# Performance work log

Measured on AMD Instinct MI355X. Metric: run time of the kernel, lower is better.

## Reference

```python
import jax, jax.numpy as jnp
import numpy as np

BS, H = 2048, 1024
XDIM = 2048 + 4 * 64  # x + R*W = 2304
IN = XDIM + 2 * H     # 4352


def setup_inputs() -> dict:
    key = jax.random.key(0)
    ks = jax.random.split(key, 11)
    s = 1.0 / np.sqrt(IN)  # torch Linear default init scale
    return {
        "input_x": jax.random.normal(ks[0], (BS, XDIM), jnp.float32),
        "previous_time": jax.random.normal(ks[1], (BS, H), jnp.float32),
        "previous_layer": jax.random.normal(ks[2], (BS, H), jnp.float32),
        "old_state": jnp.zeros((BS, H), jnp.float32),
        "Wi": jax.random.normal(ks[3], (H, IN), jnp.float32) * s,
        "bi": jax.random.normal(ks[4], (H,), jnp.float32) * s,
        "Wf": jax.random.normal(ks[5], (H, IN), jnp.float32) * s,
        "bf": jax.random.normal(ks[6], (H,), jnp.float32) * s,
        "Wo": jax.random.normal(ks[7], (H, IN), jnp.float32) * s,
        "bo": jax.random.normal(ks[8], (H,), jnp.float32) * s,
        "Ws": jax.random.normal(ks[9], (H, IN), jnp.float32) * s,
        "bs_state": jax.random.normal(ks[10], (H,), jnp.float32) * s,
    }


def reference(input_x, previous_time, previous_layer, old_state,
              Wi, bi, Wf, bf, Wo, bo, Ws, bs_state):
    # semicolon_input: [bs, x + R*W + 2h]
    z = jnp.concatenate([input_x, previous_time, previous_layer], axis=1)
    # Fuse the four projections into one GEMM: [bs, 4h]
    W_all = jnp.concatenate([Wi, Wf, Wo, Ws], axis=0)          # [4h, IN]
    b_all = jnp.concatenate([bi, bf, bo, bs_state], axis=0)    # [4h]
    proj = z @ W_all.T + b_all
    gi, gf, go, gs = jnp.split(proj, 4, axis=1)
    input_gate = jax.nn.sigmoid(gi)
    forget_gate = jax.nn.sigmoid(gf)
    output_gate = jax.nn.sigmoid(go)
    new_state = forget_gate * old_state + input_gate * jnp.tanh(gs)
    new_hidden = output_gate * jnp.tanh(new_state)
    return new_hidden
```

## Files before the change

kernel.cpp:

```cpp
#include <hip/hip_runtime.h>
#include <stdint.h>
#include <stddef.h>

#define M_DIM 2048
#define N_DIM 4096
#define K_DIM 4352
#define H_DIM 1024
#define X_DIM 2304

#define A_OFF 0u
#define B_OFF 17825792u

typedef __bf16 bf16x8 __attribute__((ext_vector_type(8)));
typedef float f32x4 __attribute__((ext_vector_type(4)));

__device__ __forceinline__ unsigned short f32_to_bf16(float f) {
    unsigned u = __float_as_uint(f);
    u += 0x7FFFu + ((u >> 16) & 1u);
    return (unsigned short)(u >> 16);
}

__device__ __forceinline__ float sigm_(float x) { return 1.f / (1.f + __expf(-x)); }
__device__ __forceinline__ float tanh_(float x) {
    x = fminf(15.f, fmaxf(-15.f, x));
    float e = __expf(2.f * x);
    return (e - 1.f) / (e + 1.f);
}

__global__ __launch_bounds__(256) void convert_kernel(
    const float* __restrict__ x, const float* __restrict__ pt,
    const float* __restrict__ pl,
    const float* __restrict__ Wi, const float* __restrict__ Wf,
    const float* __restrict__ Wo, const float* __restrict__ Ws,
    unsigned short* __restrict__ Abf, unsigned short* __restrict__ Bbf)
{
    const int row = blockIdx.x;
    const float* srow = nullptr;
    unsigned short* drow;
    if (row < M_DIM) {
        drow = Abf + (size_t)row * K_DIM;
    } else {
        int n = row - M_DIM;
        int g = n >> 10, h = n & 1023;
        const float* W = (g == 0) ? Wi : (g == 1) ? Wf : (g == 2) ? Wo : Ws;
        srow = W + (size_t)h * K_DIM;
        drow = Bbf + (size_t)(h * 4 + g) * K_DIM;
    }

    for (int c8 = threadIdx.x; c8 < K_DIM / 8; c8 += 256) {
        int col = c8 * 8;
        const float* s;
        if (row < M_DIM) {
            if (col < X_DIM)              s = x  + (size_t)row * X_DIM + col;
            else if (col < X_DIM + H_DIM) s = pt + (size_t)row * H_DIM + (col - X_DIM);
            else                          s = pl + (size_t)row * H_DIM + (col - X_DIM - H_DIM);
        } else {
            s = srow + col;
        }
        float4 v0 = ((const float4*)s)[0];
        float4 v1 = ((const float4*)s)[1];
        union { unsigned short h[8]; uint4 u; } r;
        r.h[0] = f32_to_bf16(v0.x); r.h[1] = f32_to_bf16(v0.y);
        r.h[2] = f32_to_bf16(v0.z); r.h[3] = f32_to_bf16(v0.w);
        r.h[4] = f32_to_bf16(v1.x); r.h[5] = f32_to_bf16(v1.y);
        r.h[6] = f32_to_bf16(v1.z); r.h[7] = f32_to_bf16(v1.w);
        *(uint4*)(drow + col) = r.u;
    }
}

__global__ __launch_bounds__(256) void gemm_fused(
    const unsigned short* __restrict__ A,
    const unsigned short* __restrict__ B,
    const float* __restrict__ old_state,
    const float* __restrict__ bi, const float* __restrict__ bfv,
    const float* __restrict__ bo, const float* __restrict__ bs,
    float* __restrict__ out)
{
    __shared__ __align__(16) char smem[65536];
    float* sP = (float*)smem;

    const int tid  = threadIdx.x;
    const int lane = tid & 63;
    const int wave = tid >> 6;
    const int wm = (wave >> 1) * 64;
    const int wn = (wave & 1) * 64;

    const int b   = blockIdx.x;
    const int xcd = b & 7;
    const int j   = b >> 3;
    const int n0  = (xcd * 4 + (j & 3)) * 128;
    const int m0  = (j >> 2) * 128;

    const int srow = wave * 8 + (lane >> 3);
    const int c8s  = ((lane & 7) ^ (lane >> 3)) * 8;

    const int fr  = lane & 15;
    const int sw  = fr & 7;
    const int kb0 = lane >> 4;

    f32x4 acc[4][4];
#pragma unroll
    for (int i = 0; i < 4; ++i)
#pragma unroll
        for (int jj = 0; jj < 4; ++jj) acc[i][jj] = (f32x4){0.f, 0.f, 0.f, 0.f};

    const unsigned short* Aw = A + (size_t)(m0 + srow) * K_DIM + c8s;
    const unsigned short* Bw = B + (size_t)(n0 + srow) * K_DIM + c8s;

    auto stage = [&](int kt, int bufOff) {
#pragma unroll
        for (int i = 0; i < 4; ++i) {
            __builtin_amdgcn_global_load_lds(
                (const __attribute__((address_space(1))) unsigned*)(Aw + (size_t)i * 32 * K_DIM + kt),
                (__attribute__((address_space(3))) unsigned*)(smem + bufOff + i * 4096 + wave * 1024),
                16, 0, 0);
            __builtin_amdgcn_global_load_lds(
                (const __attribute__((address_space(1))) unsigned*)(Bw + (size_t)i * 32 * K_DIM + kt),
                (__attribute__((address_space(3))) unsigned*)(smem + bufOff + 16384 + i * 4096 + wave * 1024),
                16, 0, 0);
        }
    };

    auto compute = [&](int bufOff) {
        const unsigned short* sA = (const unsigned short*)(smem + bufOff);
        const unsigned short* sB = (const unsigned short*)(smem + bufOff + 16384);
#pragma unroll
        for (int kk = 0; kk < 64; kk += 32) {
            const int kb = kk / 8 + kb0;
            bf16x8 af[4], bfr[4];
#pragma unroll
            for (int i = 0; i < 4; ++i) {
                const int ra  = wm + i * 16 + fr;
                const int rb_ = wn + i * 16 + fr;
                af[i]  = *(const bf16x8*)(sA + (ra  * 8 + (kb ^ sw)) * 8);
                bfr[i] = *(const bf16x8*)(sB + (rb_ * 8 + (kb ^ sw)) * 8);
            }
#pragma unroll
            for (int i = 0; i < 4; ++i)
#pragma unroll
                for (int jj = 0; jj < 4; ++jj)
                    acc[i][jj] = __builtin_amdgcn_mfma_f32_16x16x32_bf16(
                        af[i], bfr[jj], acc[i][jj], 0, 0, 0);
        }
    };

    stage(0, 0);

    for (int kt = 0; kt < K_DIM; kt += 128) {
        __syncthreads();
        if (kt + 64 < K_DIM) stage(kt + 64, 32768);
        compute(0);
        __syncthreads();
        if (kt + 128 < K_DIM) stage(kt + 128, 0);
        compute(32768);
    }

    const int cw = lane & 15;
    const int rw = (lane >> 4) * 4;
    const int hl = tid & 15;
    const int rb = tid >> 4;

    for (int p = 0; p < 2; ++p) {
        __syncthreads();
        if ((wave & 1) == p) {
#pragma unroll
            for (int i = 0; i < 4; ++i)
#pragma unroll
                for (int jj = 0; jj < 4; ++jj)
#pragma unroll
                    for (int r = 0; r < 4; ++r)
                        sP[(wm + i * 16 + rw + r) * 76 + jj * 16 + cw] = acc[i][jj][r];
        }
        __syncthreads();

        const int hg = (n0 >> 2) + p * 16 + hl;
        const float b_i = bi[hg], b_f = bfv[hg], b_o = bo[hg], b_s = bs[hg];
#pragma unroll
        for (int k = 0; k < 8; ++k) {
            const int row = rb + 16 * k;
            float4 g = *(const float4*)(sP + row * 76 + hl * 4);
            const size_t oidx = (size_t)(m0 + row) * H_DIM + hg;
            float old = old_state[oidx];
            float ig = sigm_(g.x + b_i);
            float fg = sigm_(g.y + b_f);
            float og = sigm_(g.z + b_o);
            float ts = tanh_(g.w + b_s);
            out[oidx] = og * tanh_(fg * old + ig * ts);
        }
    }
}

extern "C" void kernel_launch(void* const* d_in, const int* in_sizes, int n_in,
                              void* d_out, int out_size, void* d_ws, size_t ws_size,
                              hipStream_t stream) {
    const float* x   = (const float*)d_in[0];
    const float* pt  = (const float*)d_in[1];
    const float* pl  = (const float*)d_in[2];
    const float* old = (const float*)d_in[3];
    const float* Wi  = (const float*)d_in[4];
    const float* bi  = (const float*)d_in[5];
    const float* Wf  = (const float*)d_in[6];
    const float* bf  = (const float*)d_in[7];
    const float* Wo  = (const float*)d_in[8];
    const float* bo  = (const float*)d_in[9];
    const float* Ws  = (const float*)d_in[10];
    const float* bs  = (const float*)d_in[11];
    float* out = (float*)d_out;

    char* ws = (char*)d_ws;
    unsigned short* Abf = (unsigned short*)(ws + A_OFF);
    unsigned short* Bbf = (unsigned short*)(ws + B_OFF);

    convert_kernel<<<M_DIM + N_DIM, 256, 0, stream>>>(x, pt, pl, Wi, Wf, Wo, Ws, Abf, Bbf);

    gemm_fused<<<512, 256, 0, stream>>>(Abf, Bbf, old, bi, bf, bo, bs, out);
}
```

Measured before the change: 232.9 us.

## Restructure GEMM main loop with explicit waitcnt/barriers, occupancy hint, staggered start

The GEMM main loop now issues the next stage's global-to-LDS loads, then reads all A/B fragments for both k-halves at once and runs the MFMAs, with a manual vmcnt(0) wait and a raw s_barrier in place of __syncthreads. Launch bounds now request two blocks per CU, and half the blocks sleep briefly at start to stagger their memory traffic. The convert kernel switches from 8-wide to 4-wide vectors per thread. Holding all fragments up front raises register pressure, and the manual synchronisation depends on the hardware's load-to-LDS ordering being correct.

```diff
diff --git a/kernel.cpp b/kernel.cpp
--- a/kernel.cpp
+++ b/kernel.cpp
@@ -47,8 +47,8 @@
         drow = Bbf + (size_t)(h * 4 + g) * K_DIM;
     }
 
-    for (int c8 = threadIdx.x; c8 < K_DIM / 8; c8 += 256) {
-        int col = c8 * 8;
+    for (int c4 = threadIdx.x; c4 < K_DIM / 4; c4 += 256) {
+        int col = c4 * 4;
         const float* s;
         if (row < M_DIM) {
             if (col < X_DIM)              s = x  + (size_t)row * X_DIM + col;
@@ -57,18 +57,15 @@
         } else {
             s = srow + col;
         }
-        float4 v0 = ((const float4*)s)[0];
-        float4 v1 = ((const float4*)s)[1];
-        union { unsigned short h[8]; uint4 u; } r;
-        r.h[0] = f32_to_bf16(v0.x); r.h[1] = f32_to_bf16(v0.y);
-        r.h[2] = f32_to_bf16(v0.z); r.h[3] = f32_to_bf16(v0.w);
-        r.h[4] = f32_to_bf16(v1.x); r.h[5] = f32_to_bf16(v1.y);
-        r.h[6] = f32_to_bf16(v1.z); r.h[7] = f32_to_bf16(v1.w);
-        *(uint4*)(drow + col) = r.u;
-    }
-}
-
-__global__ __launch_bounds__(256) void gemm_fused(
+        float4 v = *(const float4*)s;
+        union { unsigned short h[4]; uint2 u; } r;
+        r.h[0] = f32_to_bf16(v.x); r.h[1] = f32_to_bf16(v.y);
+        r.h[2] = f32_to_bf16(v.z); r.h[3] = f32_to_bf16(v.w);
+        *(uint2*)(drow + col) = r.u;
+    }
+}
+
+__global__ __launch_bounds__(256, 2) void gemm_fused(
     const unsigned short* __restrict__ A,
     const unsigned short* __restrict__ B,
     const float* __restrict__ old_state,
@@ -91,69 +88,94 @@
     const int n0  = (xcd * 4 + (j & 3)) * 128;
     const int m0  = (j >> 2) * 128;
 
+    if ((b >> 8) & 1) __builtin_amdgcn_s_sleep(6);
+
     const int srow = wave * 8 + (lane >> 3);
     const int c8s  = ((lane & 7) ^ (lane >> 3)) * 8;
-
-    const int fr  = lane & 15;
-    const int sw  = fr & 7;
-    const int kb0 = lane >> 4;
-
-    f32x4 acc[4][4];
-#pragma unroll
-    for (int i = 0; i < 4; ++i)
-#pragma unroll
-        for (int jj = 0; jj < 4; ++jj) acc[i][jj] = (f32x4){0.f, 0.f, 0.f, 0.f};
-
     const unsigned short* Aw = A + (size_t)(m0 + srow) * K_DIM + c8s;
     const unsigned short* Bw = B + (size_t)(n0 + srow) * K_DIM + c8s;
 
-    auto stage = [&](int kt, int bufOff) {
+    const int fr  = lane & 15;
+    const int kb0 = lane >> 4;
+    const int sw  = fr & 7;
+    const int sK0 = ((kb0    ) ^ sw) * 16;
+    const int sK1 = ((kb0 ^ 4) ^ sw) * 16;
+    const int aRow =         (wm + fr) * 128;
+    const int bRow = 16384 + (wn + fr) * 128;
+
+    f32x4 acc[4][4];
+#pragma unroll
+    for (int i = 0; i < 4; ++i)
+#pragma unroll
+        for (int jj = 0; jj < 4; ++jj) acc[i][jj] = (f32x4){0.f, 0.f, 0.f, 0.f};
+
+    bf16x8 aF[4], aG[4], bF[4], bG[4];
+
+#define GLDS(GP, LP) __builtin_amdgcn_global_load_lds(                          \
+        (const __attribute__((address_space(1))) unsigned*)(GP),                \
+        (__attribute__((address_space(3))) unsigned*)(LP), 16, 0, 0)
+
+    auto STAGE_AB = [&](int kt, int bufOff) {
 #pragma unroll
         for (int i = 0; i < 4; ++i) {
-            __builtin_amdgcn_global_load_lds(
-                (const __attribute__((address_space(1))) unsigned*)(Aw + (size_t)i * 32 * K_DIM + kt),
-                (__attribute__((address_space(3))) unsigned*)(smem + bufOff + i * 4096 + wave * 1024),
-                16, 0, 0);
-            __builtin_amdgcn_global_load_lds(
-                (const __attribute__((address_space(1))) unsigned*)(Bw + (size_t)i * 32 * K_DIM + kt),
-                (__attribute__((address_space(3))) unsigned*)(smem + bufOff + 16384 + i * 4096 + wave * 1024),
-                16, 0, 0);
+            GLDS(Aw + (size_t)i * 32 * K_DIM + kt,
+                 smem + bufOff + i * 4096 + wave * 1024);
+            GLDS(Bw + (size_t)i * 32 * K_DIM + kt,
+                 smem + bufOff + 16384 + i * 4096 + wave * 1024);
         }
     };
 
-    auto compute = [&](int bufOff) {
-        const unsigned short* sA = (const unsigned short*)(smem + bufOff);
-        const unsigned short* sB = (const unsigned short*)(smem + bufOff + 16384);
-#pragma unroll
-        for (int kk = 0; kk < 64; kk += 32) {
-            const int kb = kk / 8 + kb0;
-            bf16x8 af[4], bfr[4];
-#pragma unroll
-            for (int i = 0; i < 4; ++i) {
-                const int ra  = wm + i * 16 + fr;
-                const int rb_ = wn + i * 16 + fr;
-                af[i]  = *(const bf16x8*)(sA + (ra  * 8 + (kb ^ sw)) * 8);
-                bfr[i] = *(const bf16x8*)(sB + (rb_ * 8 + (kb ^ sw)) * 8);
-            }
-#pragma unroll
-            for (int i = 0; i < 4; ++i)
-#pragma unroll
-                for (int jj = 0; jj < 4; ++jj)
-                    acc[i][jj] = __builtin_amdgcn_mfma_f32_16x16x32_bf16(
-                        af[i], bfr[jj], acc[i][jj], 0, 0, 0);
-        }
-    };
-
-    stage(0, 0);
-
-    for (int kt = 0; kt < K_DIM; kt += 128) {
-        __syncthreads();
-        if (kt + 64 < K_DIM) stage(kt + 64, 32768);
-        compute(0);
-        __syncthreads();
-        if (kt + 128 < K_DIM) stage(kt + 128, 0);
-        compute(32768);
-    }
+#define RD_ALL(BUF) {                                                           \
+        const char* bb_ = smem + (BUF);                                         \
+        _Pragma("unroll")                                                       \
+        for (int i_ = 0; i_ < 4; ++i_) {                                        \
+            aF[i_] = *(const bf16x8*)(bb_ + aRow + i_ * 2048 + sK0);            \
+            aG[i_] = *(const bf16x8*)(bb_ + aRow + i_ * 2048 + sK1);            \
+            bF[i_] = *(const bf16x8*)(bb_ + bRow + i_ * 2048 + sK0);            \
+            bG[i_] = *(const bf16x8*)(bb_ + bRow + i_ * 2048 + sK1);            \
+        } }
+
+#define MM_ALL                                                                  \
+    _Pragma("unroll")                                                           \
+    for (int i_ = 0; i_ < 4; ++i_)                                              \
+        _Pragma("unroll")                                                       \
+        for (int j_ = 0; j_ < 4; ++j_) {                                        \
+            acc[i_][j_] = __builtin_amdgcn_mfma_f32_16x16x32_bf16(              \
+                aF[i_], bF[j_], acc[i_][j_], 0, 0, 0);                          \
+            acc[i_][j_] = __builtin_amdgcn_mfma_f32_16x16x32_bf16(              \
+                aG[i_], bG[j_], acc[i_][j_], 0, 0, 0);                          \
+        }
+
+#define VM0 asm volatile("s_waitcnt vmcnt(0)" ::: "memory")
+
+    STAGE_AB(0, 0);
+    VM0;
+    __builtin_amdgcn_s_barrier();
+
+    for (int kt = 0; kt < 4352; kt += 128) {
+        STAGE_AB(kt + 64, 32768);
+        __builtin_amdgcn_sched_barrier(0);
+        RD_ALL(0);
+        MM_ALL;
+        VM0;
+        __builtin_amdgcn_s_barrier();
+        if (kt + 128 < 4352) {
+            STAGE_AB(kt + 128, 0);
+            __builtin_amdgcn_sched_barrier(0);
+            RD_ALL(32768);
+            MM_ALL;
+            VM0;
+        } else {
+            RD_ALL(32768);
+            MM_ALL;
+        }
+        __builtin_amdgcn_s_barrier();
+    }
+
+#undef RD_ALL
+#undef MM_ALL
+#undef VM0
+#undef GLDS
 
     const int cw = lane & 15;
     const int rw = (lane >> 4) * 4;
```

Result: no change. 232.0 us (-0.4%).
